# Optimization experiments

Measured on AMD Instinct MI355X. Metric: run time of the kernel, lower is better.

The kernel has to match this reference:

```python
import jax, jax.numpy as jnp
import numpy as np

B, N, M = 4, 2048, 2048
DIM, DIM_KEYS, DIM_OUT = 512, 512, 512
HEADS, DIM_HEAD = 8, 64
INNER = HEADS * DIM_HEAD


def setup_inputs() -> dict:
    key = jax.random.key(0)
    ks = jax.random.split(key, 9)
    x = jax.random.normal(ks[0], (B, N, DIM), dtype=jnp.float32)
    context = jax.random.normal(ks[1], (B, M, DIM_KEYS), dtype=jnp.float32)
    mask = jax.random.randint(ks[2], (B, N), 0, 2).astype(bool)
    context_mask = jax.random.randint(ks[3], (B, M), 0, 2).astype(bool)
    Wq = jax.random.normal(ks[4], (DIM, INNER), dtype=jnp.float32) * 0.02
    Wkv = jax.random.normal(ks[5], (DIM_KEYS, 2 * INNER), dtype=jnp.float32) * 0.02
    Wo = jax.random.normal(ks[6], (INNER, DIM_OUT), dtype=jnp.float32) * 0.02
    bo = jnp.zeros((DIM_OUT,), dtype=jnp.float32)
    null_key = jax.random.normal(ks[7], (DIM_HEAD,), dtype=jnp.float32)
    null_value = jax.random.normal(ks[8], (DIM_HEAD,), dtype=jnp.float32)
    return {"x": x, "context": context, "mask": mask, "context_mask": context_mask,
            "Wq": Wq, "Wkv": Wkv, "Wo": Wo, "bo": bo,
            "null_key": null_key, "null_value": null_value}


def reference(x, context, mask, context_mask, Wq, Wkv, Wo, bo, null_key, null_value):
    b, n, _ = x.shape
    m = context.shape[1]
    h, dh = HEADS, DIM_HEAD
    scale = dh ** -0.5

    # projections -> [b, h, n, dh]
    q = (x @ Wq).reshape(b, n, h, dh).transpose(0, 2, 1, 3)
    kv = context @ Wkv  # [b, m, 2*inner]
    k, v = jnp.split(kv, 2, axis=-1)
    k = k.reshape(b, m, h, dh).transpose(0, 2, 1, 3)
    v = v.reshape(b, m, h, dh).transpose(0, 2, 1, 3)

    # prepend null key/value token -> j = m + 1
    nk = jnp.broadcast_to(null_key, (b, h, 1, dh))
    nv = jnp.broadcast_to(null_value, (b, h, 1, dh))
    k = jnp.concatenate([nk, k], axis=2)
    v = jnp.concatenate([nv, v], axis=2)

    # qk activation (tanh) BEFORE the dot product
    q = jnp.tanh(q)
    k = jnp.tanh(k)

    sim = jnp.einsum('bhid,bhjd->bhij', q, k) * scale  # [b,h,n,m+1]

    # null token is always attendable -> pad context mask with True
    cm = jnp.pad(context_mask, ((0, 0), (1, 0)), constant_values=True)
    full_mask = mask[:, None, :, None] & cm[:, None, None, :]
    neg = -jnp.finfo(sim.dtype).max
    sim = jnp.where(full_mask, sim, neg)

    attn = jax.nn.softmax(sim, axis=-1)
    out = jnp.einsum('bhij,bhjd->bhid', attn, v)
    out = out.transpose(0, 2, 1, 3).reshape(b, n, h * dh)
    return out @ Wo + bo
```

## Files before the change

### kernel.cpp

```cpp
#include <hip/hip_runtime.h>
#include <math.h>

#define BB 4
#define NN 2048
#define MM 2048
#define HEADS 8
#define DH 64

typedef _Float16 f16;
typedef _Float16 f16x4 __attribute__((ext_vector_type(4)));
typedef _Float16 f16x8 __attribute__((ext_vector_type(8)));
typedef float f32x4 __attribute__((ext_vector_type(4)));
typedef unsigned short ushort;

#define LOG2E 1.44269504088896f
#define QSCALE (0.125f * LOG2E)

#if __has_builtin(__builtin_amdgcn_exp2f)
#define EXP2(x) __builtin_amdgcn_exp2f(x)
#else
#define EXP2(x) exp2f(x)
#endif

__device__ __forceinline__ f16x4 pk4(float a, float b, float c, float d) {
#if __has_builtin(__builtin_amdgcn_cvt_pkrtz)
    auto t0 = __builtin_amdgcn_cvt_pkrtz(a, b);
    auto t1 = __builtin_amdgcn_cvt_pkrtz(c, d);
    f16x4 r;
    r[0] = t0[0]; r[1] = t0[1]; r[2] = t1[0]; r[3] = t1[1];
    return r;
#else
    f16x4 r = {(f16)a, (f16)b, (f16)c, (f16)d};
    return r;
#endif
}

__device__ __forceinline__ void gl16(const void* g, void* l) {
    __builtin_amdgcn_global_load_lds(
        (const __attribute__((address_space(1))) unsigned int*)g,
        (__attribute__((address_space(3))) unsigned int*)l, 16, 0, 0);
}

__device__ __forceinline__ f16x8 cvt8(float4 lo, float4 hi) {
    f16x8 r;
    r[0] = (f16)lo.x; r[1] = (f16)lo.y; r[2] = (f16)lo.z; r[3] = (f16)lo.w;
    r[4] = (f16)hi.x; r[5] = (f16)hi.y; r[6] = (f16)hi.z; r[7] = (f16)hi.w;
    return r;
}

__global__ void wprep_k(const float* __restrict__ Wq, const float* __restrict__ Wkv,
                        const float* __restrict__ Wo,
                        f16* __restrict__ wq16, f16* __restrict__ wkv16,
                        f16* __restrict__ woh, f16* __restrict__ wol)
{
    __shared__ f16 S0[64 * 36], S1[64 * 36];
    const int tid = threadIdx.x;
    const int bid = blockIdx.x;
    const int K = 512;
    const float* W; int N; f16* T16; f16 *Th, *Tl; int id;
    if (bid < 128)      { W = Wq;  N = 512;  T16 = wq16;  Th = 0; Tl = 0; id = bid; }
    else if (bid < 384) { W = Wkv; N = 1024; T16 = wkv16; Th = 0; Tl = 0; id = bid - 128; }
    else                { W = Wo;  N = 512;  T16 = 0; Th = woh; Tl = wol; id = bid - 384; }
    const int k0 = (id & 15) * 32, n0 = (id >> 4) * 64;
    const int kr = tid >> 3, nc = (tid & 7) * 8;
    float4 v0 = *(const float4*)(W + (size_t)(k0 + kr) * N + n0 + nc);
    float4 v1 = *(const float4*)(W + (size_t)(k0 + kr) * N + n0 + nc + 4);
    float e[8] = {v0.x, v0.y, v0.z, v0.w, v1.x, v1.y, v1.z, v1.w};
    const int n = tid >> 2, kc = (tid & 3) * 8;
    if (T16) {
#pragma unroll
        for (int j = 0; j < 8; j++) S0[(nc + j) * 36 + kr] = (f16)e[j];
        __syncthreads();
        *(uint4*)(T16 + (size_t)(n0 + n) * K + k0 + kc) = *(const uint4*)(S0 + n * 36 + kc);
    } else {
#pragma unroll
        for (int j = 0; j < 8; j++) {
            f16 h = (f16)e[j];
            S0[(nc + j) * 36 + kr] = h;
            S1[(nc + j) * 36 + kr] = (f16)(e[j] - (float)h);
        }
        __syncthreads();
        *(uint4*)(Th + (size_t)(n0 + n) * K + k0 + kc) = *(const uint4*)(S0 + n * 36 + kc);
        *(uint4*)(Tl + (size_t)(n0 + n) * K + k0 + kc) = *(const uint4*)(S1 + n * 36 + kc);
    }
}

__launch_bounds__(256, 3)
__global__ void proj_k(const float* __restrict__ x, const float* __restrict__ ctx,
                       const f16* __restrict__ wq16, const f16* __restrict__ wkv16,
                       f16* __restrict__ qws, f16* __restrict__ kws, f16* __restrict__ vt)
{
    __shared__ __align__(16) char smem[16384];

    const int tid  = threadIdx.x;
    const int wave = tid >> 6, lane = tid & 63;
    const int l15  = lane & 15, quad = lane >> 4;
    const int by = blockIdx.y;
    const int isQ = (by < 4);
    const float* A32 = isQ ? x : ctx;
    const f16* Bt  = isQ ? wq16 : wkv16;
    const int c0 = (isQ ? by : by - 4) * 128;
    const size_t r0 = (size_t)blockIdx.x * 128;
    const int K = 512;

    const int blr = lane >> 2;
    const int bsw = (lane & 3) ^ ((lane >> 3) & 3);
    const char* bP = (const char*)(Bt + (size_t)(c0 + wave * 32 + blr) * K) + bsw * 16;
    char* bD = smem + wave * 2048;

    gl16(bP,          bD);
    gl16(bP + 16384,  bD + 1024);
    bP += 64;

    const float* aB0 = A32 + (r0 + wave * 32 + l15) * K + quad * 8;
    const float* aB1 = aB0 + 16 * K;
    float4 a0lo = *(const float4*)(aB0);
    float4 a0hi = *(const float4*)(aB0 + 4);
    float4 a1lo = *(const float4*)(aB1);
    float4 a1hi = *(const float4*)(aB1 + 4);
    int ak = 32;

    const int fsw = ((quad ^ ((l15 >> 1) & 3)) << 4);

    f32x4 acc[2][8] = {};

    int buf = 0;
    for (int t = 0; t < 16; t++) {
        __syncthreads();
        const int nb = (buf ^ 1) * 8192;
        if (t < 15) {
            gl16(bP,          bD + nb);
            gl16(bP + 16384,  bD + nb + 1024);
            bP += 64;
        }
        f16x8 a[2];
        a[0] = cvt8(a0lo, a0hi);
        a[1] = cvt8(a1lo, a1hi);
        if (t < 15) {
            a0lo = *(const float4*)(aB0 + ak);
            a0hi = *(const float4*)(aB0 + ak + 4);
            a1lo = *(const float4*)(aB1 + ak);
            a1hi = *(const float4*)(aB1 + ak + 4);
            ak += 32;
        }
        const char* sB = smem + buf * 8192;
#pragma unroll
        for (int half = 0; half < 2; half++) {
            f16x8 b[4];
#pragma unroll
            for (int c = 0; c < 4; c++)
                b[c] = *(const f16x8*)(sB + ((half * 4 + c) * 16 + l15) * 64 + fsw);
#pragma unroll
            for (int rt = 0; rt < 2; rt++)
#pragma unroll
                for (int c = 0; c < 4; c++)
                    acc[rt][half * 4 + c] = __builtin_amdgcn_mfma_f32_16x16x32_f16(
                        a[rt], b[c], acc[rt][half * 4 + c], 0, 0, 0);
        }
        buf ^= 1;
    }

    const int b    = (int)(r0 >> 11);
    const int rloc = ((int)(r0 & 2047)) + wave * 32;

#pragma unroll
    for (int rt = 0; rt < 2; rt++)
#pragma unroll
        for (int ct = 0; ct < 8; ct++) {
            const int col = c0 + ct * 16 + l15;
            if (isQ || col < 512) {
                const int h = (col >> 6) & 7;
                const int d = col & 63;
                f16* dst = isQ ? qws : kws;
                const float sc = isQ ? QSCALE : 1.0f;
#pragma unroll
                for (int reg = 0; reg < 4; reg++) {
                    const int nn = rloc + rt * 16 + quad * 4 + reg;
                    dst[(((size_t)b * 8 + h) * 2048 + nn) * 64 + d] =
                        (f16)(tanhf(acc[rt][ct][reg]) * sc);
                }
            } else {
                const int c = col - 512;
                const int h = c >> 6;
                const int d = c & 63;
                const int m0 = rloc + rt * 16 + quad * 4;
                f16x4 pk;
#pragma unroll
                for (int reg = 0; reg < 4; reg++) pk[reg] = (f16)acc[rt][ct][reg];
                *(f16x4*)(vt + (((size_t)b * 8 + h) * 64 + d) * 2048 + m0) = pk;
            }
        }
}

__launch_bounds__(256, 4)
__global__ void attn_k(const f16* __restrict__ qws, const f16* __restrict__ kws,
                       const f16* __restrict__ vtws,
                       const int* __restrict__ mask, const int* __restrict__ cmask,
                       const float* __restrict__ nk, const float* __restrict__ nv,
                       f16* __restrict__ Opf, float* __restrict__ lp)
{
    __shared__ __align__(16) char smem[32768];

    const int tid  = threadIdx.x;
    const int wave = tid >> 6, lane = tid & 63;
    const int l15  = lane & 15, quad = lane >> 4;
    const int bh = blockIdx.x, b = bh >> 3, h = bh & 7;
    const int q0 = blockIdx.y * 128 + wave * 32;
    const int jh = blockIdx.z;
    const int jbeg = jh << 9, jend = jbeg + 512;

    const f16* kg0 = kws + (size_t)bh * MM * DH;
    const f16* vg0 = vtws + (size_t)bh * DH * MM;

    const int lrow = lane >> 3;
    const int lsw  = ((lane & 7) ^ lrow) << 4;
    const char* kP = (const char*)kg0 + (size_t)(jbeg + wave * 16 + lrow) * 128 + lsw;
    const char* vP = (const char*)vg0 + (size_t)(wave * 16 + lrow) * 4096
                   + (size_t)jbeg * 2 + lsw;
    char* kD = smem + wave * 2048;
    char* vD = smem + 8192 + wave * 2048;

    gl16(kP,         kD);
    gl16(kP + 1024,  kD + 1024);
    gl16(vP,         vD);
    gl16(vP + 32768, vD + 1024);
    kP += 8192; vP += 128;

    f16x8 qf[2][2];
    const f16* qbase = qws + ((size_t)bh * NN + q0) * DH;
#pragma unroll
    for (int rt = 0; rt < 2; rt++)
#pragma unroll
        for (int ks = 0; ks < 2; ks++)
            qf[rt][ks] = *(const f16x8*)(qbase + (rt * 16 + l15) * DH + ks * 32 + quad * 8);

    int rowOk[2];
#pragma unroll
    for (int rt = 0; rt < 2; rt++)
        rowOk[rt] = mask[(size_t)b * NN + q0 + rt * 16 + l15];

    float pnull[2] = {0.0f, 0.0f};
    if (jh == 0) {
        float pn[2] = {0.f, 0.f};
#pragma unroll
        for (int ks = 0; ks < 2; ks++)
#pragma unroll
            for (int t = 0; t < 8; t++) {
                const float nkt = tanhf(nk[ks * 32 + quad * 8 + t]);
                pn[0] += (float)qf[0][ks][t] * nkt;
                pn[1] += (float)qf[1][ks][t] * nkt;
            }
#pragma unroll
        for (int rt = 0; rt < 2; rt++) {
            pn[rt] += __shfl_xor(pn[rt], 16);
            pn[rt] += __shfl_xor(pn[rt], 32);
            pnull[rt] = rowOk[rt] ? EXP2(pn[rt]) : 1.0f;
        }
    }
    float negsel[2];
#pragma unroll
    for (int rt = 0; rt < 2; rt++) {
        negsel[rt] = rowOk[rt] ? -1.0e30f : 0.0f;
        if (!rowOk[rt]) {
            const f16x8 zz = {(f16)0, (f16)0, (f16)0, (f16)0, (f16)0, (f16)0, (f16)0, (f16)0};
            qf[rt][0] = zz; qf[rt][1] = zz;
        }
    }

    f32x4 acc[2][4];
    f32x4 accl[2];
#pragma unroll
    for (int rt = 0; rt < 2; rt++)
#pragma unroll
        for (int reg = 0; reg < 4; reg++) {
            const float pr = __shfl(pnull[rt], quad * 4 + reg, 16);
            accl[rt][reg] = pr;
#pragma unroll
            for (int ds = 0; ds < 4; ds++)
                acc[rt][ds][reg] = pr * nv[ds * 16 + l15];
        }

    const f16x4 vone = {(f16)1, (f16)1, (f16)1, (f16)1};
    const int kxor = l15 & 7;

    __syncthreads();

    int buf = 0;
    for (int jc = jbeg; jc < jend; jc += 64) {
        int4 cmv[4];
#pragma unroll
        for (int jj = 0; jj < 4; jj++)
            cmv[jj] = *(const int4*)(cmask + (size_t)b * MM + jc + jj * 16 + quad * 4);

        if (jc + 64 < jend) {
            const int bo = (buf ^ 1) << 14;
            gl16(kP,         kD + bo);
            gl16(kP + 1024,  kD + bo + 1024);
            gl16(vP,         vD + bo);
            gl16(vP + 32768, vD + bo + 1024);
            kP += 8192; vP += 128;
        }

        const char* sKb = smem + (buf << 14);
        const char* sVb = sKb + 8192;

        f32x4 st[2][4];
#pragma unroll
        for (int rt = 0; rt < 2; rt++)
#pragma unroll
            for (int jj = 0; jj < 4; jj++) {
                st[rt][jj][0] = cmv[jj].x ? 0.0f : negsel[rt];
                st[rt][jj][1] = cmv[jj].y ? 0.0f : negsel[rt];
                st[rt][jj][2] = cmv[jj].z ? 0.0f : negsel[rt];
                st[rt][jj][3] = cmv[jj].w ? 0.0f : negsel[rt];
            }

#pragma unroll
        for (int ks = 0; ks < 2; ks++) {
            f16x8 kb[4];
#pragma unroll
            for (int jj = 0; jj < 4; jj++)
                kb[jj] = *(const f16x8*)(sKb + (jj * 16 + l15) * 128
                                             + (((ks * 4 + quad) ^ kxor) << 4));
#pragma unroll
            for (int rt = 0; rt < 2; rt++)
#pragma unroll
                for (int jj = 0; jj < 4; jj++)
                    st[rt][jj] = __builtin_amdgcn_mfma_f32_16x16x32_f16(
                        kb[jj], qf[rt][ks], st[rt][jj], 0, 0, 0);
        }

        f16x4 pa[2][4];
#pragma unroll
        for (int rt = 0; rt < 2; rt++)
#pragma unroll
            for (int jj = 0; jj < 4; jj++)
                pa[rt][jj] = pk4(EXP2(st[rt][jj][0]), EXP2(st[rt][jj][1]),
                                 EXP2(st[rt][jj][2]), EXP2(st[rt][jj][3]));

#pragma unroll
        for (int jj = 0; jj < 4; jj++) {
            f16x4 vb[4];
#pragma unroll
            for (int ds = 0; ds < 4; ds++)
                vb[ds] = *(const f16x4*)(sVb + (ds * 16 + l15) * 128
                                             + (((jj * 2 + (quad >> 1)) ^ kxor) << 4)
                                             + ((quad & 1) << 3));
#pragma unroll
            for (int rt = 0; rt < 2; rt++) {
#pragma unroll
                for (int ds = 0; ds < 4; ds++)
                    acc[rt][ds] = __builtin_amdgcn_mfma_f32_16x16x16f16(
                        pa[rt][jj], vb[ds], acc[rt][ds], 0, 0, 0);
                accl[rt] = __builtin_amdgcn_mfma_f32_16x16x16f16(
                    pa[rt][jj], vone, accl[rt], 0, 0, 0);
            }
        }

        __syncthreads();
        buf ^= 1;
    }

#pragma unroll
    for (int rt = 0; rt < 2; rt++) {
        float inv[4];
#pragma unroll
        for (int reg = 0; reg < 4; reg++)
            inv[reg] = 1.0f / fmaxf(accl[rt][reg], 1e-35f);
#pragma unroll
        for (int ds = 0; ds < 4; ds++)
#pragma unroll
            for (int reg = 0; reg < 4; reg++) {
                const int r = q0 + rt * 16 + quad * 4 + reg;
                Opf[((size_t)jh * 8192 + b * 2048 + r) * 512 + h * 64 + ds * 16 + l15] =
                    (f16)(acc[rt][ds][reg] * inv[reg]);
            }
    }
    if (l15 == 0) {
#pragma unroll
        for (int rt = 0; rt < 2; rt++)
#pragma unroll
            for (int reg = 0; reg < 4; reg++)
                lp[((size_t)jh * 32 + bh) * 2048 + q0 + rt * 16 + quad * 4 + reg] =
                    accl[rt][reg];
    }
}

__global__ void merge_k(const f16* __restrict__ Opf, const float* __restrict__ lp,
                        f16* __restrict__ of16)
{
    const int i = blockIdx.x * 256 + threadIdx.x;
    const int row = i >> 7;
    const int c4  = i & 127;
    const int b = row >> 11, n = row & 2047, h = c4 >> 4;
    float w[4], den = 0.f;
#pragma unroll
    for (int jh = 0; jh < 4; jh++) {
        w[jh] = lp[((size_t)jh * 32 + b * 8 + h) * 2048 + n];
        den += w[jh];
    }
    const float inv = 1.0f / den;
    float v0 = 0, v1 = 0, v2 = 0, v3 = 0;
#pragma unroll
    for (int jh = 0; jh < 4; jh++) {
        f16x4 o = *(const f16x4*)(Opf + ((size_t)jh * 8192 + row) * 512 + c4 * 4);
        v0 += (float)o[0] * w[jh];
        v1 += (float)o[1] * w[jh];
        v2 += (float)o[2] * w[jh];
        v3 += (float)o[3] * w[jh];
    }
    f16x4 r = pk4(v0 * inv, v1 * inv, v2 * inv, v3 * inv);
    *(f16x4*)(of16 + (size_t)row * 512 + c4 * 4) = r;
}

__launch_bounds__(256, 4)
__global__ void mgemm2(const f16* __restrict__ A, const f16* __restrict__ Bh,
                       const f16* __restrict__ Bl,
                       float* __restrict__ o32, const float* __restrict__ bias,
                       int K)
{
    __shared__ __align__(16) char smem[16384];

    const int tid  = threadIdx.x;
    const int wave = tid >> 6, lane = tid & 63;
    const int l15  = lane & 15, quad = lane >> 4;
    const size_t r0 = (size_t)blockIdx.x * 128;
    const int c0 = blockIdx.y * 64;

    const int blr = lane >> 2;
    const int bsw = (lane & 3) ^ ((lane >> 3) & 3);
    const char* hP = (const char*)(Bh + (size_t)(c0 + wave * 16 + blr) * K) + bsw * 16;
    const char* lP = (const char*)(Bl + (size_t)(c0 + wave * 16 + blr) * K) + bsw * 16;
    char* hD = smem + wave * 1024;
    char* lD = smem + 4096 + wave * 1024;

    gl16(hP, hD);
    gl16(lP, lD);
    hP += 64; lP += 64;

    const f16* aB0 = A + (r0 + wave * 32 + l15) * K + quad * 8;
    const f16* aB1 = aB0 + 16 * K;
    f16x8 a0 = *(const f16x8*)(aB0);
    f16x8 a1 = *(const f16x8*)(aB1);
    int ak = 32;

    const int fsw = ((quad ^ ((l15 >> 1) & 3)) << 4);

    f32x4 acc[2][4] = {};

    int buf = 0;
    const int NT = K / 32;
    for (int t = 0; t < NT; t++) {
        __syncthreads();
        const int nb = (buf ^ 1) * 8192;
        if (t < NT - 1) {
            gl16(hP, hD + nb);
            gl16(lP, lD + nb);
            hP += 64; lP += 64;
        }
        f16x8 ca0 = a0, ca1 = a1;
        if (t < NT - 1) {
            a0 = *(const f16x8*)(aB0 + ak);
            a1 = *(const f16x8*)(aB1 + ak);
            ak += 32;
        }
        const char* sH = smem + buf * 8192;
        const char* sL = sH + 4096;
#pragma unroll
        for (int ct = 0; ct < 4; ct++) {
            const int boff = (ct * 16 + l15) * 64 + fsw;
            f16x8 bh = *(const f16x8*)(sH + boff);
            f16x8 bl = *(const f16x8*)(sL + boff);
            acc[0][ct] = __builtin_amdgcn_mfma_f32_16x16x32_f16(ca0, bh, acc[0][ct], 0, 0, 0);
            acc[0][ct] = __builtin_amdgcn_mfma_f32_16x16x32_f16(ca0, bl, acc[0][ct], 0, 0, 0);
            acc[1][ct] = __builtin_amdgcn_mfma_f32_16x16x32_f16(ca1, bh, acc[1][ct], 0, 0, 0);
            acc[1][ct] = __builtin_amdgcn_mfma_f32_16x16x32_f16(ca1, bl, acc[1][ct], 0, 0, 0);
        }
        buf ^= 1;
    }

#pragma unroll
    for (int rt = 0; rt < 2; rt++)
#pragma unroll
        for (int ct = 0; ct < 4; ct++) {
            const int col = c0 + ct * 16 + l15;
            const float bv = bias[col];
#pragma unroll
            for (int reg = 0; reg < 4; reg++) {
                const size_t row = r0 + wave * 32 + rt * 16 + quad * 4 + reg;
                o32[row * 512 + col] = acc[rt][ct][reg] + bv;
            }
        }
}

extern "C" void kernel_launch(void* const* d_in, const int* in_sizes, int n_in,
                              void* d_out, int out_size, void* d_ws, size_t ws_size,
                              hipStream_t stream)
{
    const float* x    = (const float*)d_in[0];
    const float* ctx  = (const float*)d_in[1];
    const int*   mask = (const int*)d_in[2];
    const int*   cmsk = (const int*)d_in[3];
    const float* Wq   = (const float*)d_in[4];
    const float* Wkv  = (const float*)d_in[5];
    const float* Wo   = (const float*)d_in[6];
    const float* bo   = (const float*)d_in[7];
    const float* nk   = (const float*)d_in[8];
    const float* nv   = (const float*)d_in[9];
    float* out = (float*)d_out;

    const size_t S = (size_t)BB * HEADS * NN * DH;

    f16* qws = (f16*)d_ws;
    f16* kws = qws + S;
    f16* vt  = kws + S;
    f16* wq16  = vt + S;
    f16* wkv16 = wq16 + 512 * 512;
    f16* woh = wkv16 + 512 * 1024;
    f16* wol = woh + 512 * 512;
    float* lp = (float*)(wol + 512 * 512);
    f16* Opf = (f16*)(lp + 4 * 32 * 2048);
    f16* of16 = qws;

    wprep_k<<<512, 256, 0, stream>>>(Wq, Wkv, Wo, wq16, wkv16, woh, wol);
    proj_k<<<dim3(64, 12), 256, 0, stream>>>(x, ctx, wq16, wkv16, qws, kws, vt);
    attn_k<<<dim3(32, 16, 4), 256, 0, stream>>>(qws, kws, vt, mask, cmsk, nk, nv, Opf, lp);
    merge_k<<<4096, 256, 0, stream>>>(Opf, lp, of16);
    mgemm2<<<dim3(64, 8), 256, 0, stream>>>(of16, woh, wol, out, bo, 512);
}
```

Before: 206.2 us.

## Halve attention key-splits and stage output-GEMM A tiles through LDS

The attention kernel now splits the key range into two chunks of 1024 instead of four chunks of 512, and the merge kernel combines two partials instead of four. This halves partial-output traffic and merge work, at the cost of fewer blocks (1024) and longer per-block loops. Separately, the output GEMM now loads its A operand into double-buffered shared memory via async copies instead of direct per-lane global loads. It also moves the barrier to the end of each iteration, which doubles LDS use per block.

```diff
diff --git a/kernel.cpp b/kernel.cpp
--- a/kernel.cpp
+++ b/kernel.cpp
@@ -207,7 +207,7 @@
     const int bh = blockIdx.x, b = bh >> 3, h = bh & 7;
     const int q0 = blockIdx.y * 128 + wave * 32;
     const int jh = blockIdx.z;
-    const int jbeg = jh << 9, jend = jbeg + 512;
+    const int jbeg = jh << 10, jend = jbeg + 1024;
 
     const f16* kg0 = kws + (size_t)bh * MM * DH;
     const f16* vg0 = vtws + (size_t)bh * DH * MM;
@@ -393,16 +393,16 @@
     const int row = i >> 7;
     const int c4  = i & 127;
     const int b = row >> 11, n = row & 2047, h = c4 >> 4;
-    float w[4], den = 0.f;
-#pragma unroll
-    for (int jh = 0; jh < 4; jh++) {
+    float w[2], den = 0.f;
+#pragma unroll
+    for (int jh = 0; jh < 2; jh++) {
         w[jh] = lp[((size_t)jh * 32 + b * 8 + h) * 2048 + n];
         den += w[jh];
     }
     const float inv = 1.0f / den;
     float v0 = 0, v1 = 0, v2 = 0, v3 = 0;
 #pragma unroll
-    for (int jh = 0; jh < 4; jh++) {
+    for (int jh = 0; jh < 2; jh++) {
         f16x4 o = *(const f16x4*)(Opf + ((size_t)jh * 8192 + row) * 512 + c4 * 4);
         v0 += (float)o[0] * w[jh];
         v1 += (float)o[1] * w[jh];
@@ -419,7 +419,7 @@
                        float* __restrict__ o32, const float* __restrict__ bias,
                        int K)
 {
-    __shared__ __align__(16) char smem[16384];
+    __shared__ __align__(16) char smem[32768];
 
     const int tid  = threadIdx.x;
     const int wave = tid >> 6, lane = tid & 63;
@@ -429,53 +429,58 @@
 
     const int blr = lane >> 2;
     const int bsw = (lane & 3) ^ ((lane >> 3) & 3);
+    const char* aP = (const char*)(A + (r0 + wave * 32 + blr) * K) + bsw * 16;
     const char* hP = (const char*)(Bh + (size_t)(c0 + wave * 16 + blr) * K) + bsw * 16;
     const char* lP = (const char*)(Bl + (size_t)(c0 + wave * 16 + blr) * K) + bsw * 16;
-    char* hD = smem + wave * 1024;
-    char* lD = smem + 4096 + wave * 1024;
-
-    gl16(hP, hD);
-    gl16(lP, lD);
-    hP += 64; lP += 64;
-
-    const f16* aB0 = A + (r0 + wave * 32 + l15) * K + quad * 8;
-    const f16* aB1 = aB0 + 16 * K;
-    f16x8 a0 = *(const f16x8*)(aB0);
-    f16x8 a1 = *(const f16x8*)(aB1);
-    int ak = 32;
+    char* aD = smem + wave * 2048;
+    char* hD = smem + 8192 + wave * 1024;
+    char* lD = smem + 12288 + wave * 1024;
+
+    gl16(aP,          aD);
+    gl16(aP + 16384,  aD + 1024);
+    gl16(hP,          hD);
+    gl16(lP,          lD);
+    aP += 64; hP += 64; lP += 64;
 
     const int fsw = ((quad ^ ((l15 >> 1) & 3)) << 4);
+    const int aoff0 = (wave * 32 + l15) * 64 + fsw;
+    const int aoff1 = aoff0 + 16 * 64;
 
     f32x4 acc[2][4] = {};
+    __syncthreads();
 
     int buf = 0;
     const int NT = K / 32;
     for (int t = 0; t < NT; t++) {
-        __syncthreads();
-        const int nb = (buf ^ 1) * 8192;
+        const int nb = (buf ^ 1) * 16384;
         if (t < NT - 1) {
-            gl16(hP, hD + nb);
-            gl16(lP, lD + nb);
-            hP += 64; lP += 64;
-        }
-        f16x8 ca0 = a0, ca1 = a1;
-        if (t < NT - 1) {
-            a0 = *(const f16x8*)(aB0 + ak);
-            a1 = *(const f16x8*)(aB1 + ak);
-            ak += 32;
-        }
-        const char* sH = smem + buf * 8192;
-        const char* sL = sH + 4096;
+            gl16(aP,          aD + nb);
+            gl16(aP + 16384,  aD + nb + 1024);
+            gl16(hP,          hD + nb);
+            gl16(lP,          lD + nb);
+            aP += 64; hP += 64; lP += 64;
+        }
+        const char* sA = smem + buf * 16384;
+        const char* sH = sA + 8192;
+        const char* sL = sA + 12288;
+
+        f16x8 a[2];
+        a[0] = *(const f16x8*)(sA + aoff0);
+        a[1] = *(const f16x8*)(sA + aoff1);
 #pragma unroll
         for (int ct = 0; ct < 4; ct++) {
             const int boff = (ct * 16 + l15) * 64 + fsw;
             f16x8 bh = *(const f16x8*)(sH + boff);
             f16x8 bl = *(const f16x8*)(sL + boff);
-            acc[0][ct] = __builtin_amdgcn_mfma_f32_16x16x32_f16(ca0, bh, acc[0][ct], 0, 0, 0);
-            acc[0][ct] = __builtin_amdgcn_mfma_f32_16x16x32_f16(ca0, bl, acc[0][ct], 0, 0, 0);
-            acc[1][ct] = __builtin_amdgcn_mfma_f32_16x16x32_f16(ca1, bh, acc[1][ct], 0, 0, 0);
-            acc[1][ct] = __builtin_amdgcn_mfma_f32_16x16x32_f16(ca1, bl, acc[1][ct], 0, 0, 0);
-        }
+#pragma unroll
+            for (int rt = 0; rt < 2; rt++) {
+                acc[rt][ct] = __builtin_amdgcn_mfma_f32_16x16x32_f16(
+                    a[rt], bh, acc[rt][ct], 0, 0, 0);
+                acc[rt][ct] = __builtin_amdgcn_mfma_f32_16x16x32_f16(
+                    a[rt], bl, acc[rt][ct], 0, 0, 0);
+            }
+        }
+        __syncthreads();
         buf ^= 1;
     }
 
@@ -524,7 +529,7 @@
 
     wprep_k<<<512, 256, 0, stream>>>(Wq, Wkv, Wo, wq16, wkv16, woh, wol);
     proj_k<<<dim3(64, 12), 256, 0, stream>>>(x, ctx, wq16, wkv16, qws, kws, vt);
-    attn_k<<<dim3(32, 16, 4), 256, 0, stream>>>(qws, kws, vt, mask, cmsk, nk, nv, Opf, lp);
+    attn_k<<<dim3(32, 16, 2), 256, 0, stream>>>(qws, kws, vt, mask, cmsk, nk, nv, Opf, lp);
     merge_k<<<4096, 256, 0, stream>>>(Opf, lp, of16);
     mgemm2<<<dim3(64, 8), 256, 0, stream>>>(of16, woh, wol, out, bo, 512);
 }
```

Result: faster. 195.1 us (-5.4%).
